# Optimization experiments

Hardware: AMD Instinct MI355X
Metric: run time of the kernel (lower is better)

Reference implementation:

```python
import jax, jax.numpy as jnp
import numpy as np

ALPHA = 0.2   # LeakyReLU slope
V = 7         # graph nodes (hard-coded 7x7 adjacency in source)
BN_EPS = 1e-5


def _leaky(x):
    return jnp.where(x >= 0, x, ALPHA * x)


def _norm_adj(B):
    # adj = min-max normalized (B + I), then D^{-1/2} adj D^{-1/2}
    adj = B + jnp.eye(V, dtype=B.dtype)
    adj = (adj - adj.min()) / (adj.max() - adj.min())
    inv = 1.0 / jnp.sqrt(jnp.sum(adj, axis=1))
    return adj * inv[:, None] * inv[None, :]


def _gat1_head(h_flat, W, a, B):
    # h_flat: (N, V, C*T)=  (N,7,180); W: (180,9); a: (18,1); B: (7,7)
    Wh = h_flat @ W                       # (N, V, E)
    E = W.shape[1]
    s_i = Wh @ a[:E, 0]                   # (N, V)  == [Wh_i ; .] part of concat score
    s_j = Wh @ a[E:, 0]                   # (N, V)  == [. ; Wh_j] part
    e = _leaky(s_i[:, :, None] + s_j[:, None, :])   # (N, V, V)
    att = jax.nn.softmax(e, axis=-1)
    adjn = _norm_adj(B)
    att = jnp.einsum('ik,nkj->nij', adjn, att)      # adj_norm @ attention
    return jax.nn.elu(att @ Wh)           # (N, V, E)


def _gat2_head(h, W, a, B):
    # h: (N, V, C, 30); W: (30,10); a: (20,1); B: (7,7)
    Wh = h @ W                            # (N, V, C, F)
    F = W.shape[1]
    s_i = jnp.einsum('nvcf,f->nvc', Wh, a[:F, 0])
    s_j = jnp.einsum('nvcf,f->nvc', Wh, a[F:, 0])
    e = _leaky(s_i[:, :, None, :] + s_j[:, None, :, :])   # (N, V, V, C)
    att = jax.nn.softmax(e, axis=-1)      # softmax over channel dim (as in source)
    # nested V-loop with diag_embed == weighted sum over j, per-channel scaling
    h2 = jnp.einsum('njcf,nijc->ncfi', Wh, att)           # (N, C, F, V)
    adjn = _norm_adj(B)
    out = jnp.einsum('ncfu,uv->ncfv', h2, adjn)
    return jax.nn.elu(out)                # (N, C, F, V)


def setup_inputs() -> dict:
    key = jax.random.key(0)
    ks = jax.random.split(key, 16)
    N, C, T = 32768, 6, 30
    f32 = jnp.float32
    inp = {
        'x': jax.random.normal(ks[0], (N, C, T, V), f32),
        'bn_gamma': jax.random.uniform(ks[1], (42,), f32, 0.5, 1.5),
        'bn_beta': 0.1 * jax.random.normal(ks[2], (42,), f32),
        'W1': 0.1 * jax.random.normal(ks[3], (20, 180, 9), f32),
        'a1': 0.1 * jax.random.normal(ks[4], (20, 18, 1), f32),
        'B1': 0.01 * jax.random.uniform(ks[5], (20, V, V), f32) + 1e-6,
        'W2': 0.1 * jax.random.normal(ks[6], (3, 30, 10), f32),
        'a2': 0.1 * jax.random.normal(ks[7], (3, 20, 1), f32),
        'B2': 0.01 * jax.random.uniform(ks[8], (3, V, V), f32) + 1e-6,
        'W_ih': 0.1 * jax.random.normal(ks[9], (84, 84), f32),
        'W_hh': 0.1 * jax.random.normal(ks[10], (84, 21), f32),
        'b_ih': 0.1 * jax.random.normal(ks[11], (84,), f32),
        'b_hh': 0.1 * jax.random.normal(ks[12], (84,), f32),
        'W_out': 0.1 * jax.random.normal(ks[13], (7, 21), f32),
        'b_out': 0.1 * jax.random.normal(ks[14], (7,), f32),
    }
    return inp


def reference(x, bn_gamma, bn_beta, W1, a1, B1, W2, a2, B2,
              W_ih, W_hh, b_ih, b_hh, W_out, b_out):
    N, C, T, _ = x.shape                  # (N, 6, 30, 7)
    # data_bn: BatchNorm1d(42) in train mode (batch stats over N and T)
    xb = jnp.transpose(x, (0, 3, 1, 2)).reshape(N, V * C, T)
    mean = jnp.mean(xb, axis=(0, 2), keepdims=True)
    var = jnp.var(xb, axis=(0, 2), keepdims=True)
    xb = (xb - mean) / jnp.sqrt(var + BN_EPS)
    xb = xb * bn_gamma[None, :, None] + bn_beta[None, :, None]
    x0 = jnp.transpose(xb.reshape(N, V, C, T), (0, 2, 3, 1))   # (N, C, T, V)

    # l1: 20-head GAT on flattened (C*T) node features
    h_flat = jnp.transpose(x0, (0, 3, 1, 2)).reshape(N, V, C * T)
    heads1 = jax.vmap(_gat1_head, in_axes=(None, 0, 0, 0))(h_flat, W1, a1, B1)  # (20,N,V,9)
    x1 = jnp.moveaxis(heads1, 0, 2).reshape(N, V, C * T)       # cat over heads, last dim
    x1 = jnp.transpose(x1.reshape(N, V, C, T), (0, 2, 3, 1))   # (N, C, T, V)

    # l2: 3-head 2D GAT over the T axis
    h2in = jnp.transpose(x0, (0, 3, 1, 2))                      # (N, V, C, T)
    heads2 = jax.vmap(_gat2_head, in_axes=(None, 0, 0, 0))(h2in, W2, a2, B2)  # (3,N,C,10,V)
    x2 = jnp.moveaxis(heads2, 0, 2).reshape(N, C, 30, V)        # cat over heads on dim=2

    xcat = jnp.concatenate([x1, x2], axis=1)                    # (N, 12, 30, 7)

    # RNN head: source takes r_out[:, 0, :], so only LSTM step 0 (h0=c0=0) matters
    xs = jnp.transpose(xcat, (0, 2, 1, 3)).reshape(N, T, 84)
    gates = xs[:, 0, :] @ W_ih.T + b_ih + b_hh                  # h0=0 => W_hh term vanishes
    i_g, f_g, g_g, o_g = jnp.split(gates, 4, axis=-1)           # torch gate order i,f,g,o
    c1 = jax.nn.sigmoid(i_g) * jnp.tanh(g_g)
    h1 = jax.nn.sigmoid(o_g) * jnp.tanh(c1)
    return h1 @ W_out.T + b_out                                 # (N, 7)
```

## Files before the change

### kernel.cpp

```cpp
#include <hip/hip_runtime.h>

#define F1260 1260
#define NPART 128
#define PB_OFF 10752

__device__ __forceinline__ float leakyf(float x) { return x >= 0.f ? x : 0.2f * x; }
__device__ __forceinline__ float eluf(float x) { return x > 0.f ? x : expm1f(x); }
__device__ __forceinline__ float sigmoidf(float x) { return 1.f / (1.f + __expf(-x)); }
__device__ __forceinline__ float tanh_fast(float x) { return 1.f - 2.f / (__expf(2.f * x) + 1.f); }


__global__ __launch_bounds__(320) void kA_stats(const float* __restrict__ x,
                                                float* __restrict__ ws, int rows) {
    __shared__ float fs[1260], fq[1260];
    const int t = threadIdx.x;
    const int n0 = blockIdx.x * rows;
    if (t < 315) {
        const int f0 = t * 4;
        float s0 = 0.f, s1 = 0.f, s2 = 0.f, s3 = 0.f;
        float q0 = 0.f, q1 = 0.f, q2 = 0.f, q3 = 0.f;
#pragma unroll 16
        for (int i = 0; i < rows; ++i) {
            const float4 a = *(const float4*)(x + (size_t)(n0 + i) * F1260 + f0);
            s0 += a.x; q0 += a.x * a.x;
            s1 += a.y; q1 += a.y * a.y;
            s2 += a.z; q2 += a.z * a.z;
            s3 += a.w; q3 += a.w * a.w;
        }
        fs[f0 + 0] = s0; fq[f0 + 0] = q0;
        fs[f0 + 1] = s1; fq[f0 + 1] = q1;
        fs[f0 + 2] = s2; fq[f0 + 2] = q2;
        fs[f0 + 3] = s3; fq[f0 + 3] = q3;
    }
    __syncthreads();
    if (t < 42) {
        const int v = t / 6, c = t % 6;
        float s = 0.f, q = 0.f;
#pragma unroll
        for (int tt = 0; tt < 30; ++tt) {
            const int f = c * 210 + tt * 7 + v;
            s += fs[f];
            q += fq[f];
        }
        ws[blockIdx.x * 84 + t] = s;
        ws[blockIdx.x * 84 + 42 + t] = q;
    }
}

__global__ __launch_bounds__(256) void kB_setup(
        const float* __restrict__ bn_gamma, const float* __restrict__ bn_beta,
        const float* __restrict__ W1, const float* __restrict__ a1, const float* __restrict__ B1,
        const float* __restrict__ W2, const float* __restrict__ a2, const float* __restrict__ B2,
        const float* __restrict__ b_ih, const float* __restrict__ b_hh,
        const float* __restrict__ W_out, const float* __restrict__ b_out,
        float* __restrict__ ws, int N) {
    const int t = threadIdx.x;
    float* pb = ws + PB_OFF;
    const int HH[6] = {0, 3, 6, 10, 13, 16};
    const int EH[6] = {0, 3, 6, 0, 3, 6};

    if (t < 42) {
        float s = 0.f, q = 0.f;
        for (int b = 0; b < NPART; ++b) {
            s += ws[b * 84 + t];
            q += ws[b * 84 + 42 + t];
        }
        const float cnt = 30.f * (float)N;
        const float mean = s / cnt;
        const float var = q / cnt - mean * mean;
        const float sc = bn_gamma[t] * rsqrtf(var + 1e-5f);
        pb[t] = sc;
        pb[64 + t] = bn_beta[t] - mean * sc;
    }
    if (t >= 64 && t < 71) {
        const int idx = t - 64;
        const float* Bp = (idx < 6) ? (B1 + HH[idx] * 49) : B2;
        float* op = pb + 128 + idx * 49;
        float adj[49];
        for (int i = 0; i < 49; ++i) adj[i] = Bp[i];
        for (int i = 0; i < 7; ++i) adj[i * 8] += 1.f;
        float mn = adj[0], mx = adj[0];
        for (int i = 1; i < 49; ++i) { mn = fminf(mn, adj[i]); mx = fmaxf(mx, adj[i]); }
        const float inv = 1.f / (mx - mn);
        float rinv[7];
        for (int i = 0; i < 7; ++i) {
            float rs = 0.f;
            for (int j = 0; j < 7; ++j) { adj[i * 7 + j] = (adj[i * 7 + j] - mn) * inv; rs += adj[i * 7 + j]; }
            rinv[i] = rsqrtf(rs);
        }
        for (int i = 0; i < 7; ++i)
            for (int j = 0; j < 7; ++j)
                op[i * 7 + j] = adj[i * 7 + j] * rinv[i] * rinv[j];
    }
    for (int task = t; task < 6 * 180; task += 256) {
        const int hh = task / 180, k = task % 180;
        const int h = HH[hh];
        const float* Wp = W1 + ((size_t)h * 180 + k) * 9;
        float si = 0.f, sj = 0.f;
        for (int e = 0; e < 9; ++e) {
            const float w = Wp[e];
            si += w * a1[h * 18 + e];
            sj += w * a1[h * 18 + 9 + e];
        }
        pb[512 + k * 24 + hh * 3 + 0] = si;
        pb[512 + k * 24 + hh * 3 + 1] = sj;
        pb[512 + k * 24 + hh * 3 + 2] = Wp[EH[hh]];
    }
    if (t < 30) {
        const float* Wp = W2 + t * 10;
        float si = 0.f, sj = 0.f;
        for (int f = 0; f < 10; ++f) {
            const float w = Wp[f];
            si += w * a2[f];
            sj += w * a2[10 + f];
        }
        for (int c = 0; c < 6; ++c) {
            const int k = c * 30 + t;
            pb[512 + k * 24 + 18] = si;
            pb[512 + k * 24 + 19] = sj;
            pb[512 + k * 24 + 20] = Wp[0];
        }
    }
    if (t < 84) pb[4832 + t] = b_ih[t] + b_hh[t];
    if (t < 147) pb[4928 + t] = W_out[t];
    if (t < 7) pb[5078 + t] = b_out[t];
}

#define RS 252
__global__ __launch_bounds__(64) void kC_main(const float* __restrict__ x,
        const float* __restrict__ pb, const float* __restrict__ Wih,
        float* __restrict__ outp, int N) {
    __shared__ __align__(16) float sm[3627];
    float* res  = sm;
    float* xs0  = sm + 2016;
    float* h2t  = sm + 2688;
    float* h1s  = sm + 3024;
    float* scsh = sm + 3200;
    float* adjL = sm + 3284;

    const int t = threadIdx.x;
    const int n0 = blockIdx.x * 8;

    for (int i = t; i < 84; i += 64) scsh[i] = pb[i < 42 ? i : 22 + i];
    for (int i = t; i < 343; i += 64) adjL[i] = pb[128 + i];
    __syncthreads();

    const int v = t >> 3, nl = t & 7;
    if (v < 7) {
        float s1[18];
#pragma unroll
        for (int i = 0; i < 18; ++i) s1[i] = 0.f;
        const float* xb = x + (size_t)(n0 + nl) * F1260 + v;
        const float* WB = pb + 512;
        for (int c = 0; c < 6; ++c) {
            const float sc = scsh[v * 6 + c];
            const float sh = scsh[42 + v * 6 + c];
            const float* xr = xb + c * 210;
            const float* wb = WB + (c * 30) * 24;
            float xv[30];
#pragma unroll
            for (int tt = 0; tt < 30; ++tt) xv[tt] = xr[tt * 7];
            float g0 = 0.f, g1 = 0.f, g2 = 0.f;
#pragma unroll
            for (int tt = 0; tt < 30; ++tt) {
                const float a = xv[tt] * sc + sh;
                const float* w = wb + tt * 24;
#pragma unroll
                for (int q = 0; q < 18; ++q) s1[q] += a * w[q];
                g0 += a * w[18];
                g1 += a * w[19];
                g2 += a * w[20];
            }
            float* rp = res + nl * RS + 126 + (v * 6 + c) * 3;
            rp[0] = g0; rp[1] = g1; rp[2] = g2;
        }
#pragma unroll
        for (int q = 0; q < 18; ++q)
            res[nl * RS + v * 18 + q] = s1[q];
    }
    __syncthreads();

    if (t < 48) {
        const int hh = t >> 3, nl2 = t & 7;
        float si[7], sj[7], we[7];
#pragma unroll
        for (int vv = 0; vv < 7; ++vv) {
            const float* rp = res + nl2 * RS + vv * 18 + hh * 3;
            si[vv] = rp[0]; sj[vv] = rp[1]; we[vv] = rp[2];
        }
        float mxsj = sj[0];
#pragma unroll
        for (int j = 1; j < 7; ++j) mxsj = fmaxf(mxsj, sj[j]);
        float p[7];
#pragma unroll
        for (int i = 0; i < 7; ++i) {
            const float m = leakyf(si[i] + mxsj);
            float den = 0.f, num = 0.f;
#pragma unroll
            for (int j = 0; j < 7; ++j) {
                const float w = __expf(leakyf(si[i] + sj[j]) - m);
                den += w;
                num += w * we[j];
            }
            p[i] = num / den;
        }
        const float* An = adjL + hh * 49;
#pragma unroll
        for (int i = 0; i < 7; ++i) {
            float r = 0.f;
#pragma unroll
            for (int k = 0; k < 7; ++k) r += An[i * 7 + k] * p[k];
            xs0[nl2 * 84 + hh * 7 + i] = eluf(r);
        }
    }
    if (t < 56) {
        const int i = t >> 3, nl2 = t & 7;
        float si2[6];
#pragma unroll
        for (int c = 0; c < 6; ++c)
            si2[c] = res[nl2 * RS + 126 + (i * 6 + c) * 3];
        float hc[6];
#pragma unroll
        for (int c = 0; c < 6; ++c) hc[c] = 0.f;
#pragma unroll
        for (int j = 0; j < 7; ++j) {
            float s[6];
            float m = -1e30f;
#pragma unroll
            for (int c = 0; c < 6; ++c) {
                const float* rp = res + nl2 * RS + 126 + (j * 6 + c) * 3;
                s[c] = leakyf(si2[c] + rp[1]);
                m = fmaxf(m, s[c]);
            }
            float den = 0.f;
#pragma unroll
            for (int c = 0; c < 6; ++c) { s[c] = __expf(s[c] - m); den += s[c]; }
            const float rd = 1.f / den;
#pragma unroll
            for (int c = 0; c < 6; ++c) {
                const float wh0 = res[nl2 * RS + 126 + (j * 6 + c) * 3 + 2];
                hc[c] += wh0 * s[c] * rd;
            }
        }
#pragma unroll
        for (int c = 0; c < 6; ++c)
            h2t[nl2 * 42 + i * 6 + c] = hc[c];
    }
    __syncthreads();

    if (t < 48) {
        const int c = t >> 3, nl2 = t & 7;
        const float* An2 = adjL + 6 * 49;
        float h[7];
#pragma unroll
        for (int u = 0; u < 7; ++u) h[u] = h2t[nl2 * 42 + u * 6 + c];
#pragma unroll
        for (int vv = 0; vv < 7; ++vv) {
            float r = 0.f;
#pragma unroll
            for (int u = 0; u < 7; ++u) r += h[u] * An2[u * 7 + vv];
            xs0[nl2 * 84 + 42 + c * 7 + vv] = eluf(r);
        }
    }
    __syncthreads();

    {
        const int g8 = t >> 3, nl2 = t & 7;
        const float* bias = pb + 4832;
        const float4* xs4 = (const float4*)(xs0 + nl2 * 84);
        for (int gi = g8; gi < 21; gi += 8) {
            float ga = bias[gi], gg = bias[42 + gi], go = bias[63 + gi];
            const float4* wa = (const float4*)(Wih + gi * 84);
            const float4* wg = (const float4*)(Wih + (42 + gi) * 84);
            const float4* wo = (const float4*)(Wih + (63 + gi) * 84);
#pragma unroll
            for (int k = 0; k < 21; ++k) {
                const float4 xv = xs4[k];
                const float4 a4 = wa[k];
                const float4 g4 = wg[k];
                const float4 o4 = wo[k];
                ga += xv.x * a4.x + xv.y * a4.y + xv.z * a4.z + xv.w * a4.w;
                gg += xv.x * g4.x + xv.y * g4.y + xv.z * g4.z + xv.w * g4.w;
                go += xv.x * o4.x + xv.y * o4.y + xv.z * o4.z + xv.w * o4.w;
            }
            const float c1 = sigmoidf(ga) * tanh_fast(gg);
            h1s[nl2 * 22 + gi] = sigmoidf(go) * tanh_fast(c1);
        }
    }
    __syncthreads();

    if (t < 56) {
        const int nl2 = t / 7, j = t - nl2 * 7;
        const float* Wout = pb + 4928;
        float r = pb[5078 + j];
#pragma unroll
        for (int m = 0; m < 21; ++m) r += h1s[nl2 * 22 + m] * Wout[j * 21 + m];
        outp[(size_t)n0 * 7 + t] = r;
    }
}

extern "C" void kernel_launch(void* const* d_in, const int* in_sizes, int n_in,
                              void* d_out, int out_size, void* d_ws, size_t ws_size,
                              hipStream_t stream) {
    const int N = in_sizes[0] / F1260;

    const float* x        = (const float*)d_in[0];
    const float* bn_gamma = (const float*)d_in[1];
    const float* bn_beta  = (const float*)d_in[2];
    const float* W1       = (const float*)d_in[3];
    const float* a1       = (const float*)d_in[4];
    const float* B1       = (const float*)d_in[5];
    const float* W2       = (const float*)d_in[6];
    const float* a2       = (const float*)d_in[7];
    const float* B2       = (const float*)d_in[8];
    const float* W_ih     = (const float*)d_in[9];
    const float* b_ih     = (const float*)d_in[11];
    const float* b_hh     = (const float*)d_in[12];
    const float* W_out    = (const float*)d_in[13];
    const float* b_out    = (const float*)d_in[14];

    float* wsf = (float*)d_ws;


    kA_stats<<<dim3(NPART), dim3(320), 0, stream>>>(x, wsf, N / NPART);
    kB_setup<<<dim3(1), dim3(256), 0, stream>>>(bn_gamma, bn_beta, W1, a1, B1,
                                                W2, a2, B2, b_ih, b_hh,
                                                W_out, b_out, wsf, N);
    kC_main<<<dim3(N / 8), dim3(64), 0, stream>>>(x, wsf + PB_OFF, W_ih, (float*)d_out, N);
}
```

Baseline: 368.5 us.

## Process 16 samples per 128-thread block and reuse one shared buffer

The main kernel now runs 128 threads per block and handles 16 samples instead of 8, halving the grid. Separate shared arrays for intermediates are folded into the per-sample result buffer, with an extra barrier added so the attention inputs are read before being overwritten. The goal is better wave utilisation and less per-block setup overhead, at the cost of more shared memory per block and some added synchronisation.

```diff
diff --git a/kernel.cpp b/kernel.cpp
--- a/kernel.cpp
+++ b/kernel.cpp
@@ -2,7 +2,7 @@
 
 #define F1260 1260
 #define NPART 128
-#define PB_OFF 10752
+#define PB_OFF (NPART * 84)
 
 __device__ __forceinline__ float leakyf(float x) { return x >= 0.f ? x : 0.2f * x; }
 __device__ __forceinline__ float eluf(float x) { return x > 0.f ? x : expm1f(x); }
@@ -127,25 +127,23 @@
 }
 
 #define RS 252
-__global__ __launch_bounds__(64) void kC_main(const float* __restrict__ x,
+__global__ __launch_bounds__(128) void kC_main(const float* __restrict__ x,
         const float* __restrict__ pb, const float* __restrict__ Wih,
         float* __restrict__ outp, int N) {
-    __shared__ __align__(16) float sm[3627];
+    __shared__ __align__(16) float sm[4459];
     float* res  = sm;
-    float* xs0  = sm + 2016;
-    float* h2t  = sm + 2688;
-    float* h1s  = sm + 3024;
-    float* scsh = sm + 3200;
-    float* adjL = sm + 3284;
+    float* scsh = sm + 4032;
+    float* adjL = sm + 4116;
 
     const int t = threadIdx.x;
-    const int n0 = blockIdx.x * 8;
-
-    for (int i = t; i < 84; i += 64) scsh[i] = pb[i < 42 ? i : 22 + i];
-    for (int i = t; i < 343; i += 64) adjL[i] = pb[128 + i];
-    __syncthreads();
-
-    const int v = t >> 3, nl = t & 7;
+    const int n0 = blockIdx.x * 16;
+    const int v = (t >> 3) & 7;
+    const int nl = ((t >> 6) << 3) + (t & 7);
+
+    for (int i = t; i < 84; i += 128) scsh[i] = pb[i < 42 ? i : 22 + i];
+    for (int i = t; i < 343; i += 128) adjL[i] = pb[128 + i];
+    __syncthreads();
+
     if (v < 7) {
         float s1[18];
 #pragma unroll
@@ -180,14 +178,15 @@
     }
     __syncthreads();
 
-    if (t < 48) {
-        const int hh = t >> 3, nl2 = t & 7;
-        float si[7], sj[7], we[7];
-#pragma unroll
-        for (int vv = 0; vv < 7; ++vv) {
-            const float* rp = res + nl2 * RS + vv * 18 + hh * 3;
-            si[vv] = rp[0]; sj[vv] = rp[1]; we[vv] = rp[2];
-        }
+    const int hh = v;
+    float si[7], sj[7], we[7];
+#pragma unroll
+    for (int vv = 0; vv < 7; ++vv) {
+        const float* rp = res + nl * RS + vv * 18 + hh * 3;
+        si[vv] = rp[0]; sj[vv] = rp[1]; we[vv] = rp[2];
+    }
+    __syncthreads();
+    if (hh < 6) {
         float mxsj = sj[0];
 #pragma unroll
         for (int j = 1; j < 7; ++j) mxsj = fmaxf(mxsj, sj[j]);
@@ -210,15 +209,15 @@
             float r = 0.f;
 #pragma unroll
             for (int k = 0; k < 7; ++k) r += An[i * 7 + k] * p[k];
-            xs0[nl2 * 84 + hh * 7 + i] = eluf(r);
-        }
-    }
-    if (t < 56) {
-        const int i = t >> 3, nl2 = t & 7;
+            res[nl * RS + hh * 7 + i] = eluf(r);
+        }
+    }
+    if (v < 7) {
+        const int i = v;
         float si2[6];
 #pragma unroll
         for (int c = 0; c < 6; ++c)
-            si2[c] = res[nl2 * RS + 126 + (i * 6 + c) * 3];
+            si2[c] = res[nl * RS + 126 + (i * 6 + c) * 3];
         float hc[6];
 #pragma unroll
         for (int c = 0; c < 6; ++c) hc[c] = 0.f;
@@ -228,7 +227,7 @@
             float m = -1e30f;
 #pragma unroll
             for (int c = 0; c < 6; ++c) {
-                const float* rp = res + nl2 * RS + 126 + (j * 6 + c) * 3;
+                const float* rp = res + nl * RS + 126 + (j * 6 + c) * 3;
                 s[c] = leakyf(si2[c] + rp[1]);
                 m = fmaxf(m, s[c]);
             }
@@ -238,36 +237,36 @@
             const float rd = 1.f / den;
 #pragma unroll
             for (int c = 0; c < 6; ++c) {
-                const float wh0 = res[nl2 * RS + 126 + (j * 6 + c) * 3 + 2];
+                const float wh0 = res[nl * RS + 126 + (j * 6 + c) * 3 + 2];
                 hc[c] += wh0 * s[c] * rd;
             }
         }
 #pragma unroll
         for (int c = 0; c < 6; ++c)
-            h2t[nl2 * 42 + i * 6 + c] = hc[c];
-    }
-    __syncthreads();
-
-    if (t < 48) {
-        const int c = t >> 3, nl2 = t & 7;
+            res[nl * RS + 84 + i * 6 + c] = hc[c];
+    }
+    __syncthreads();
+
+    if (v < 6) {
+        const int c = v;
         const float* An2 = adjL + 6 * 49;
         float h[7];
 #pragma unroll
-        for (int u = 0; u < 7; ++u) h[u] = h2t[nl2 * 42 + u * 6 + c];
+        for (int u = 0; u < 7; ++u) h[u] = res[nl * RS + 84 + u * 6 + c];
 #pragma unroll
         for (int vv = 0; vv < 7; ++vv) {
             float r = 0.f;
 #pragma unroll
             for (int u = 0; u < 7; ++u) r += h[u] * An2[u * 7 + vv];
-            xs0[nl2 * 84 + 42 + c * 7 + vv] = eluf(r);
+            res[nl * RS + 42 + c * 7 + vv] = eluf(r);
         }
     }
     __syncthreads();
 
     {
-        const int g8 = t >> 3, nl2 = t & 7;
+        const int g8 = v + ((t >> 3) & 8 ? 0 : 0);
         const float* bias = pb + 4832;
-        const float4* xs4 = (const float4*)(xs0 + nl2 * 84);
+        const float4* xs4 = (const float4*)(res + nl * RS);
         for (int gi = g8; gi < 21; gi += 8) {
             float ga = bias[gi], gg = bias[42 + gi], go = bias[63 + gi];
             const float4* wa = (const float4*)(Wih + gi * 84);
@@ -284,17 +283,17 @@
                 go += xv.x * o4.x + xv.y * o4.y + xv.z * o4.z + xv.w * o4.w;
             }
             const float c1 = sigmoidf(ga) * tanh_fast(gg);
-            h1s[nl2 * 22 + gi] = sigmoidf(go) * tanh_fast(c1);
-        }
-    }
-    __syncthreads();
-
-    if (t < 56) {
-        const int nl2 = t / 7, j = t - nl2 * 7;
+            res[nl * RS + 126 + gi] = sigmoidf(go) * tanh_fast(c1);
+        }
+    }
+    __syncthreads();
+
+    if (t < 112) {
+        const int n5 = t / 7, j = t - n5 * 7;
         const float* Wout = pb + 4928;
         float r = pb[5078 + j];
 #pragma unroll
-        for (int m = 0; m < 21; ++m) r += h1s[nl2 * 22 + m] * Wout[j * 21 + m];
+        for (int m = 0; m < 21; ++m) r += res[n5 * RS + 126 + m] * Wout[j * 21 + m];
         outp[(size_t)n0 * 7 + t] = r;
     }
 }
@@ -326,5 +325,5 @@
     kB_setup<<<dim3(1), dim3(256), 0, stream>>>(bn_gamma, bn_beta, W1, a1, B1,
                                                 W2, a2, B2, b_ih, b_hh,
                                                 W_out, b_out, wsf, N);
-    kC_main<<<dim3(N / 8), dim3(64), 0, stream>>>(x, wsf + PB_OFF, W_ih, (float*)d_out, N);
+    kC_main<<<dim3(N / 16), dim3(128), 0, stream>>>(x, wsf + PB_OFF, W_ih, (float*)d_out, N);
 }
```

Result: faster. 337.2 us (-8.5%).
